# Kernel optimization log

Hardware: AMD Instinct MI355X
Metric: run time of the kernel (lower is better)

Reference implementation:

```python
import jax, jax.numpy as jnp
import numpy as np

EPSILON = 0.05
MAX_ITER = 50
ALPHA = 6.0
THRESHOLD = 0.25
SCALE = 0.02  # keeps OT costs near THRESHOLD so the gate is not saturated


def setup_inputs() -> dict:
    key = jax.random.key(0)
    k1, k2 = jax.random.split(key)
    B, E, D, P = 8192, 8, 512, 32
    tokens = jax.random.normal(k1, (B, E, D), dtype=jnp.float32) * SCALE
    prototypes = jax.random.normal(k2, (E, P, D), dtype=jnp.float32) * SCALE
    return {"tokens": tokens, "prototypes": prototypes, "full_index": 0}


def _sinkhorn_log(cost, epsilon, max_iter):
    # cost: [..., n_source, n_target]; batched log-domain Sinkhorn, fixed iterations
    ns, nt = cost.shape[-2], cost.shape[-1]
    log_mu = jnp.full(cost.shape[:-1], -float(np.log(ns)), dtype=cost.dtype)
    log_nu = jnp.full(cost.shape[:-2] + (nt,), -float(np.log(nt)), dtype=cost.dtype)
    log_k = -cost / epsilon

    def step(carry, _):
        log_u, log_v = carry
        log_u = log_mu - jax.scipy.special.logsumexp(log_k + log_v[..., None, :], axis=-1)
        log_v = log_nu - jax.scipy.special.logsumexp(log_k + log_u[..., :, None], axis=-2)
        return (log_u, log_v), None

    (log_u, log_v), _ = jax.lax.scan(
        step, (jnp.zeros_like(log_mu), jnp.zeros_like(log_nu)), None, length=max_iter
    )
    return jnp.exp(log_k + log_u[..., :, None] + log_v[..., None, :])


def reference(tokens, prototypes, full_index):
    # tokens: [B, E, D], prototypes: [E, P, D]
    B, E, D = tokens.shape
    anchor = tokens[:, full_index, :]                                   # [B, D]
    source = jnp.stack(
        [tokens, jnp.broadcast_to(anchor[:, None, :], tokens.shape)], axis=2
    )                                                                   # [B, E, 2, D]
    # squared euclidean cdist: ||s||^2 - 2 s.p + ||p||^2
    s2 = jnp.sum(source * source, axis=-1)                              # [B, E, 2]
    p2 = jnp.sum(prototypes * prototypes, axis=-1)                      # [E, P]
    cross = jnp.einsum('besd,epd->besp', source, prototypes)            # [B, E, 2, P]
    cost = jnp.maximum(s2[..., None] - 2.0 * cross + p2[None, :, None, :], 0.0)
    transport = _sinkhorn_log(cost, EPSILON, MAX_ITER)                  # [B, E, 2, P]
    ot_cost = jnp.sum(transport * cost, axis=(-1, -2))                  # [B, E]
    validity = jax.nn.sigmoid(-ALPHA * (ot_cost - THRESHOLD))[..., None]  # [B, E, 1]
    # the full_index expert always passes with validity 1 and zero cost
    is_full = jnp.arange(E) == full_index                               # [E]
    ot_cost = jnp.where(is_full[None, :], 0.0, ot_cost)
    validity = jnp.where(is_full[None, :, None], 1.0, validity)
    return validity, ot_cost
```

## Files before the change

### kernel.cpp

```cpp
#include <hip/hip_runtime.h>
#include <hip/hip_bf16.h>


#define EXP2F(x) __builtin_amdgcn_exp2f(x)
#define LOG2F(x) __builtin_amdgcn_logf(x)
#define RCPF(x)  __builtin_amdgcn_rcpf(x)

typedef __bf16 bf16x8 __attribute__((ext_vector_type(8)));
typedef float  f32x4  __attribute__((ext_vector_type(4)));

#define BDIM 8192
#define EDIM 8
#define DDIM 512
#define PDIM 32
#define BPB  32
#define NTHR 256
#define PFD  4
#define C_SCALE 28.853900817779268f
#define LOG2E   1.4426950408889634f

__device__ __forceinline__ bf16x8 cvt2(float4 a, float4 b) {
  bf16x8 r;
  r[0] = (__bf16)a.x; r[1] = (__bf16)a.y; r[2] = (__bf16)a.z; r[3] = (__bf16)a.w;
  r[4] = (__bf16)b.x; r[5] = (__bf16)b.y; r[6] = (__bf16)b.z; r[7] = (__bf16)b.w;
  return r;
}

__global__ __launch_bounds__(NTHR, 3)
void ot_noise_gate_kernel(const float* __restrict__ tokens,
                          const float* __restrict__ protos,
                          const int*   __restrict__ fullIndexPtr,
                          float*       __restrict__ out) {
  const int fi    = fullIndexPtr[0];
  const int e     = blockIdx.x & (EDIM - 1);
  const int b0    = (blockIdx.x >> 3) * BPB;
  float* outVal = out;
  float* outOt  = out + BDIM * EDIM;

  if (e == fi) {
    int t = threadIdx.x;
    if (t < BPB) {
      int b = b0 + t;
      outVal[b * EDIM + e] = 1.0f;
      outOt [b * EDIM + e] = 0.0f;
    }
    return;
  }

  __shared__ __align__(16) __bf16 sB[64 * PDIM * 8];
  __shared__ float sPNp[8][PDIM];
  __shared__ __align__(16) float sCw[4][16][36];

  const int t  = threadIdx.x;
  const int l  = t & 63;
  const int w  = t >> 6;
  const int fr = l & 15;
  const int q4 = l >> 4;

  const int bRow = b0 + 8 * w + (fr & 7);
  const int eSel = (fr < 8) ? e : fi;
  const float4* rp4 = (const float4*)(tokens + ((size_t)bRow * EDIM + eSel) * DDIM);

  float4 buf[PFD][2];
  #pragma unroll
  for (int c = 0; c < PFD; ++c) {
    buf[c][0] = rp4[c * 8 + q4 * 2];
    buf[c][1] = rp4[c * 8 + q4 * 2 + 1];
  }

  {
    const float4* pG4 = (const float4*)(protos + (size_t)e * PDIM * DDIM);
    const int p  = t & 31;
    const int oh = t >> 5;
    float pnp = 0.f;
    #pragma unroll
    for (int pass = 0; pass < 8; ++pass) {
      int oct = oh * 8 + pass;
      float4 a = pG4[p * 128 + oct * 2];
      float4 b = pG4[p * 128 + oct * 2 + 1];
      pnp += a.x*a.x + a.y*a.y + a.z*a.z + a.w*a.w
           + b.x*b.x + b.y*b.y + b.z*b.z + b.w*b.w;
      *(bf16x8*)&sB[(oct * PDIM + p) * 8] = cvt2(a, b);
    }
    sPNp[oh][p] = pnp;
  }
  __syncthreads();

  f32x4 acc0 = (f32x4){0.f, 0.f, 0.f, 0.f};
  f32x4 acc1 = (f32x4){0.f, 0.f, 0.f, 0.f};
  float ss = 0.f;

  #pragma unroll
  for (int kc = 0; kc < 16; ++kc) {
    float4 ca0 = buf[kc % PFD][0];
    float4 ca1 = buf[kc % PFD][1];
    if (kc < 16 - PFD) {
      buf[kc % PFD][0] = rp4[(kc + PFD) * 8 + q4 * 2];
      buf[kc % PFD][1] = rp4[(kc + PFD) * 8 + q4 * 2 + 1];
    }
    ss += ca0.x*ca0.x + ca0.y*ca0.y + ca0.z*ca0.z + ca0.w*ca0.w
        + ca1.x*ca1.x + ca1.y*ca1.y + ca1.z*ca1.z + ca1.w*ca1.w;
    bf16x8 aF  = cvt2(ca0, ca1);
    bf16x8 bF0 = *(const bf16x8*)&sB[((kc * 4 + q4) * PDIM + fr) * 8];
    bf16x8 bF1 = *(const bf16x8*)&sB[((kc * 4 + q4) * PDIM + 16 + fr) * 8];
    acc0 = __builtin_amdgcn_mfma_f32_16x16x32_bf16(aF, bF0, acc0, 0, 0, 0);
    acc1 = __builtin_amdgcn_mfma_f32_16x16x32_bf16(aF, bF1, acc1, 0, 0, 0);
  }

  ss += __shfl_xor(ss, 16);
  ss += __shfl_xor(ss, 32);
  float pn_a = 0.f, pn_b = 0.f;
  #pragma unroll
  for (int o = 0; o < 8; ++o) {
    pn_a += sPNp[o][fr];
    pn_b += sPNp[o][16 + fr];
  }

  #pragma unroll
  for (int reg = 0; reg < 4; ++reg) {
    int row = q4 * 4 + reg;
    float nrm = __shfl(ss, row);
    sCw[w][row][fr]      = fmaxf(nrm - 2.f * acc0[reg] + pn_a, 0.f);
    sCw[w][row][16 + fr] = fmaxf(nrm - 2.f * acc1[reg] + pn_b, 0.f);
  }

  const int i = l & 7;
  const int s = l >> 3;
  float c0[4], c1[4];
  {
    float4 v0 = *(const float4*)&sCw[w][i][4 * s];
    float4 v1 = *(const float4*)&sCw[w][8 + i][4 * s];
    c0[0] = v0.x; c0[1] = v0.y; c0[2] = v0.z; c0[3] = v0.w;
    c1[0] = v1.x; c1[1] = v1.y; c1[2] = v1.z; c1[3] = v1.w;
  }

  float W[4], dc[4];
  float sum0 = 0.f, mA = -1e30f, mB = -1e30f;
  #pragma unroll
  for (int r = 0; r < 4; ++r) {
    float ka = -c0[r] * C_SCALE, kb = -c1[r] * C_SCALE;
    dc[r] = c1[r] - c0[r];
    sum0 += c0[r];
    mA = fmaxf(mA, ka);
    mB = fmaxf(mB, kb);
  }
  mA = fmaxf(mA, __shfl_xor(mA, 8));
  mA = fmaxf(mA, __shfl_xor(mA, 16));
  mA = fmaxf(mA, __shfl_xor(mA, 32));
  mB = fmaxf(mB, __shfl_xor(mB, 8));
  mB = fmaxf(mB, __shfl_xor(mB, 16));
  mB = fmaxf(mB, __shfl_xor(mB, 32));
  float sa = 0.f, sb = 0.f;
  #pragma unroll
  for (int r = 0; r < 4; ++r) {
    float ka = -c0[r] * C_SCALE, kb = -c1[r] * C_SCALE;
    sa += EXP2F(ka - mA);
    sb += EXP2F(kb - mB);
    W[r] = EXP2F(C_SCALE * dc[r]);
  }
  sa += __shfl_xor(sa, 8);  sa += __shfl_xor(sa, 16);  sa += __shfl_xor(sa, 32);
  sb += __shfl_xor(sb, 8);  sb += __shfl_xor(sb, 16);  sb += __shfl_xor(sb, 32);
  sum0 += __shfl_xor(sum0, 8);
  sum0 += __shfl_xor(sum0, 16);
  sum0 += __shfl_xor(sum0, 32);
  float delta = (mB + LOG2F(sb)) - (mA + LOG2F(sa));

  for (int it = 0; it < 49; ++it) {
    float s2 = EXP2F(delta);
    float T = 0.f;
    #pragma unroll
    for (int r = 0; r < 4; ++r)
      T += RCPF(__builtin_fmaf(W[r], s2, 1.0f));
    T += __shfl_xor(T, 8);
    T += __shfl_xor(T, 16);
    T += __shfl_xor(T, 32);
    float upd = LOG2F(T) - LOG2F(32.0f - T);
    delta += upd;
    if (__ballot(fabsf(upd) > 5e-7f) == 0ull) break;
  }

  float s2 = EXP2F(delta), sv = 0.f;
  #pragma unroll
  for (int r = 0; r < 4; ++r)
    sv += RCPF(__builtin_fmaf(W[r], s2, 1.0f)) * dc[r];
  sv += __shfl_xor(sv, 8);
  sv += __shfl_xor(sv, 16);
  sv += __shfl_xor(sv, 32);
  if (s == 0) {
    int b = b0 + 8 * w + i;
    float ot  = (sum0 + sv) * 0.03125f;
    float val = RCPF(1.0f + EXP2F(LOG2E * 6.0f * (ot - 0.25f)));
    outVal[b * EDIM + e] = val;
    outOt [b * EDIM + e] = ot;
  }
}

extern "C" void kernel_launch(void* const* d_in, const int* in_sizes, int n_in,
                              void* d_out, int out_size, void* d_ws, size_t ws_size,
                              hipStream_t stream) {
  const float* tokens = (const float*)d_in[0];
  const float* protos = (const float*)d_in[1];
  const int*   fidx   = (const int*)d_in[2];
  float* out = (float*)d_out;

  dim3 grid((BDIM / BPB) * EDIM);
  ot_noise_gate_kernel<<<grid, NTHR, 0, stream>>>(tokens, protos, fidx, out);
}
```

Baseline: 206.4 us.

## Split fused kernel into cost GEMM kernel and separate Sinkhorn kernel via workspace

Splits the single fused kernel into two launches. The first computes the cost matrices with MFMA and writes them to a global workspace. The second runs the Sinkhorn iterations with two threads per problem, so reductions need a single shuffle and each wave's early-exit ballot covers 32 problems instead of 8. It also doubles the token prefetch depth. This trades an extra launch and a workspace round trip for less shuffle overhead and better-balanced iteration in the Sinkhorn phase, but the larger ballot groups may hold converged problems longer and register pressure rises.

Result: slower. 214.2 us (+3.8%).

```diff
diff --git a/kernel.cpp b/kernel.cpp
--- a/kernel.cpp
+++ b/kernel.cpp
@@ -15,7 +15,8 @@
 #define PDIM 32
 #define BPB  32
 #define NTHR 256
-#define PFD  4
+#define PFD  8
+#define TSTR 68
 #define C_SCALE 28.853900817779268f
 #define LOG2E   1.4426950408889634f
 
@@ -27,29 +28,18 @@
 }
 
 __global__ __launch_bounds__(NTHR, 3)
-void ot_noise_gate_kernel(const float* __restrict__ tokens,
-                          const float* __restrict__ protos,
-                          const int*   __restrict__ fullIndexPtr,
-                          float*       __restrict__ out) {
-  const int fi    = fullIndexPtr[0];
-  const int e     = blockIdx.x & (EDIM - 1);
-  const int b0    = (blockIdx.x >> 3) * BPB;
-  float* outVal = out;
-  float* outOt  = out + BDIM * EDIM;
-
-  if (e == fi) {
-    int t = threadIdx.x;
-    if (t < BPB) {
-      int b = b0 + t;
-      outVal[b * EDIM + e] = 1.0f;
-      outOt [b * EDIM + e] = 0.0f;
-    }
-    return;
-  }
+void cost_kernel(const float* __restrict__ tokens,
+                 const float* __restrict__ protos,
+                 const int*   __restrict__ fullIndexPtr,
+                 float*       __restrict__ wsC) {
+  const int fi = fullIndexPtr[0];
+  const int e  = blockIdx.x & (EDIM - 1);
+  const int b0 = (blockIdx.x >> 3) * BPB;
+  if (e == fi) return;
 
   __shared__ __align__(16) __bf16 sB[64 * PDIM * 8];
   __shared__ float sPNp[8][PDIM];
-  __shared__ __align__(16) float sCw[4][16][36];
+  __shared__ __align__(16) float sT[4][8][TSTR];
 
   const int t  = threadIdx.x;
   const int l  = t & 63;
@@ -118,62 +108,91 @@
 
   #pragma unroll
   for (int reg = 0; reg < 4; ++reg) {
-    int row = q4 * 4 + reg;
+    int row  = q4 * 4 + reg;
+    int prob = row & 7;
+    int half = row >> 3;
     float nrm = __shfl(ss, row);
-    sCw[w][row][fr]      = fmaxf(nrm - 2.f * acc0[reg] + pn_a, 0.f);
-    sCw[w][row][16 + fr] = fmaxf(nrm - 2.f * acc1[reg] + pn_b, 0.f);
-  }
-
-  const int i = l & 7;
-  const int s = l >> 3;
-  float c0[4], c1[4];
+    sT[w][prob][half * 32 + fr]      = fmaxf(nrm - 2.f * acc0[reg] + pn_a, 0.f);
+    sT[w][prob][half * 32 + 16 + fr] = fmaxf(nrm - 2.f * acc1[reg] + pn_b, 0.f);
+  }
+
   {
-    float4 v0 = *(const float4*)&sCw[w][i][4 * s];
-    float4 v1 = *(const float4*)&sCw[w][8 + i][4 * s];
-    c0[0] = v0.x; c0[1] = v0.y; c0[2] = v0.z; c0[3] = v0.w;
-    c1[0] = v1.x; c1[1] = v1.y; c1[2] = v1.z; c1[3] = v1.w;
-  }
-
-  float W[4], dc[4];
+    const size_t pbBase = (size_t)e * BDIM + b0 + 8 * w;
+    const int prob = l >> 3;
+    const int seg  = l & 7;
+    float4 v0 = *(const float4*)&sT[w][prob][seg * 8];
+    float4 v1 = *(const float4*)&sT[w][prob][seg * 8 + 4];
+    float4* dst = (float4*)(wsC + (pbBase + prob) * 64 + seg * 8);
+    dst[0] = v0;
+    dst[1] = v1;
+  }
+}
+
+__global__ __launch_bounds__(NTHR, 6)
+void sinkhorn_kernel(const float* __restrict__ wsC,
+                     const int*   __restrict__ fullIndexPtr,
+                     float*       __restrict__ out) {
+  const int fi = fullIndexPtr[0];
+  const int t  = threadIdx.x;
+  const int pb = blockIdx.x * (NTHR / 2) + (t >> 1);
+  const int h  = t & 1;
+  const int e  = pb >> 13;
+  const int b  = pb & (BDIM - 1);
+  float* outVal = out;
+  float* outOt  = out + BDIM * EDIM;
+
+  if (e == fi) {
+    if (h == 0) {
+      outVal[b * EDIM + e] = 1.0f;
+      outOt [b * EDIM + e] = 0.0f;
+    }
+    return;
+  }
+
+  float c0[16], c1[16];
+  {
+    const float4* base = (const float4*)(wsC + (size_t)pb * 64);
+    #pragma unroll
+    for (int r = 0; r < 4; ++r) {
+      float4 v0 = base[h * 4 + r];
+      float4 v1 = base[8 + h * 4 + r];
+      c0[4*r] = v0.x; c0[4*r+1] = v0.y; c0[4*r+2] = v0.z; c0[4*r+3] = v0.w;
+      c1[4*r] = v1.x; c1[4*r+1] = v1.y; c1[4*r+2] = v1.z; c1[4*r+3] = v1.w;
+    }
+  }
+
+  float W[16], dc[16];
   float sum0 = 0.f, mA = -1e30f, mB = -1e30f;
   #pragma unroll
-  for (int r = 0; r < 4; ++r) {
+  for (int r = 0; r < 16; ++r) {
     float ka = -c0[r] * C_SCALE, kb = -c1[r] * C_SCALE;
     dc[r] = c1[r] - c0[r];
     sum0 += c0[r];
     mA = fmaxf(mA, ka);
     mB = fmaxf(mB, kb);
   }
-  mA = fmaxf(mA, __shfl_xor(mA, 8));
-  mA = fmaxf(mA, __shfl_xor(mA, 16));
-  mA = fmaxf(mA, __shfl_xor(mA, 32));
-  mB = fmaxf(mB, __shfl_xor(mB, 8));
-  mB = fmaxf(mB, __shfl_xor(mB, 16));
-  mB = fmaxf(mB, __shfl_xor(mB, 32));
+  mA = fmaxf(mA, __shfl_xor(mA, 1));
+  mB = fmaxf(mB, __shfl_xor(mB, 1));
   float sa = 0.f, sb = 0.f;
   #pragma unroll
-  for (int r = 0; r < 4; ++r) {
+  for (int r = 0; r < 16; ++r) {
     float ka = -c0[r] * C_SCALE, kb = -c1[r] * C_SCALE;
     sa += EXP2F(ka - mA);
     sb += EXP2F(kb - mB);
     W[r] = EXP2F(C_SCALE * dc[r]);
   }
-  sa += __shfl_xor(sa, 8);  sa += __shfl_xor(sa, 16);  sa += __shfl_xor(sa, 32);
-  sb += __shfl_xor(sb, 8);  sb += __shfl_xor(sb, 16);  sb += __shfl_xor(sb, 32);
-  sum0 += __shfl_xor(sum0, 8);
-  sum0 += __shfl_xor(sum0, 16);
-  sum0 += __shfl_xor(sum0, 32);
+  sa += __shfl_xor(sa, 1);
+  sb += __shfl_xor(sb, 1);
+  sum0 += __shfl_xor(sum0, 1);
   float delta = (mB + LOG2F(sb)) - (mA + LOG2F(sa));
 
   for (int it = 0; it < 49; ++it) {
     float s2 = EXP2F(delta);
     float T = 0.f;
     #pragma unroll
-    for (int r = 0; r < 4; ++r)
+    for (int r = 0; r < 16; ++r)
       T += RCPF(__builtin_fmaf(W[r], s2, 1.0f));
-    T += __shfl_xor(T, 8);
-    T += __shfl_xor(T, 16);
-    T += __shfl_xor(T, 32);
+    T += __shfl_xor(T, 1);
     float upd = LOG2F(T) - LOG2F(32.0f - T);
     delta += upd;
     if (__ballot(fabsf(upd) > 5e-7f) == 0ull) break;
@@ -181,13 +200,10 @@
 
   float s2 = EXP2F(delta), sv = 0.f;
   #pragma unroll
-  for (int r = 0; r < 4; ++r)
+  for (int r = 0; r < 16; ++r)
     sv += RCPF(__builtin_fmaf(W[r], s2, 1.0f)) * dc[r];
-  sv += __shfl_xor(sv, 8);
-  sv += __shfl_xor(sv, 16);
-  sv += __shfl_xor(sv, 32);
-  if (s == 0) {
-    int b = b0 + 8 * w + i;
+  sv += __shfl_xor(sv, 1);
+  if (h == 0) {
     float ot  = (sum0 + sv) * 0.03125f;
     float val = RCPF(1.0f + EXP2F(LOG2E * 6.0f * (ot - 0.25f)));
     outVal[b * EDIM + e] = val;
@@ -202,7 +218,10 @@
   const float* protos = (const float*)d_in[1];
   const int*   fidx   = (const int*)d_in[2];
   float* out = (float*)d_out;
-
-  dim3 grid((BDIM / BPB) * EDIM);
-  ot_noise_gate_kernel<<<grid, NTHR, 0, stream>>>(tokens, protos, fidx, out);
-}
+  float* wsC = (float*)d_ws;
+
+  dim3 gridC((BDIM / BPB) * EDIM);
+  cost_kernel<<<gridC, NTHR, 0, stream>>>(tokens, protos, fidx, wsC);
+  dim3 gridS(BDIM * EDIM / (NTHR / 2));
+  sinkhorn_kernel<<<gridS, NTHR, 0, stream>>>(wsC, fidx, out);
+}
```
